# Kernel optimization log

Measured on AMD Instinct MI355X. Metric: run time of the kernel, lower is better.

The kernel has to match this reference:

```python
import jax, jax.numpy as jnp
import numpy as np

NUM_NODES = 50000

def setup_inputs() -> dict:
    key = jax.random.key(0)
    k1, k2 = jax.random.split(key)
    x = jax.random.normal(k1, (NUM_NODES, 64), dtype=jnp.float32)
    edge_index = jax.random.randint(k2, (2, 800000), 0, NUM_NODES, dtype=jnp.int64)
    return {"x": x, "edge_index": edge_index}

def reference(x, edge_index):
    # gather source-node features along edges, scatter-mean into target nodes
    row, col = edge_index[0], edge_index[1]
    num_nodes = x.shape[0]
    gathered = x[row]  # [E, D]
    summed = jax.ops.segment_sum(gathered, col, num_segments=num_nodes)  # [N, D]
    count = jax.ops.segment_sum(jnp.ones_like(col, dtype=x.dtype), col, num_segments=num_nodes)  # [N]
    # mean with divide-by-zero guard (matches torch_geometric scatter reduce='mean')
    out = summed / jnp.maximum(count, 1.0)[:, None]
    return out
```

## Files before the change

kernel.cpp:

```cpp
#include <hip/hip_runtime.h>

#define N_NODES 50000
#define DIM 64
#define NPB 32
#define NB 1563
#define NCHUNK 256
#define CAPB 1024
#define CAP 1024

typedef unsigned short ushort_t;

__device__ __forceinline__ ushort_t f32_to_bf16(float f) {
    unsigned u = __float_as_uint(f);
    u += 0x7FFFu + ((u >> 16) & 1u);
    return (ushort_t)(u >> 16);
}

__device__ __forceinline__ void acc_pair(float& a0, float& a1, unsigned u) {
    a0 += __uint_as_float(u << 16);
    a1 += __uint_as_float(u & 0xFFFF0000u);
}

__global__ void init_cursor_kernel(int* __restrict__ cursor) {
    int t = blockIdx.x * blockDim.x + threadIdx.x;
    if (t <= NB) cursor[t] = t * CAPB;
}

__global__ void binning_kernel(const float* __restrict__ xf,
                               ushort_t* __restrict__ xh,
                               const int* __restrict__ row,
                               const int* __restrict__ col,
                               int* __restrict__ cursor,
                               unsigned* __restrict__ packed,
                               int E, int chunk, int n4) {
    __shared__ int h[NB];
    __shared__ int lcur[NB];
    int c = blockIdx.x;
    int tid = threadIdx.x;
    for (int i = c * blockDim.x + tid; i < n4; i += gridDim.x * blockDim.x) {
        float4 v = *reinterpret_cast<const float4*>(xf + (size_t)i * 4);
        ushort4 hh;
        hh.x = f32_to_bf16(v.x);
        hh.y = f32_to_bf16(v.y);
        hh.z = f32_to_bf16(v.z);
        hh.w = f32_to_bf16(v.w);
        *reinterpret_cast<ushort4*>(xh + (size_t)i * 4) = hh;
    }
    for (int b = tid; b < NB; b += blockDim.x) h[b] = 0;
    __syncthreads();
    int beg = c * chunk, end = min(beg + chunk, E);
    int nfull = (end - beg) >> 2;
    for (int g = tid; g < nfull; g += blockDim.x) {
        int4 c4 = *reinterpret_cast<const int4*>(col + beg + g * 4);
        atomicAdd(&h[c4.x >> 5], 1);
        atomicAdd(&h[c4.y >> 5], 1);
        atomicAdd(&h[c4.z >> 5], 1);
        atomicAdd(&h[c4.w >> 5], 1);
    }
    for (int e = beg + nfull * 4 + tid; e < end; e += blockDim.x)
        atomicAdd(&h[col[e] >> 5], 1);
    __syncthreads();
    for (int b = tid; b < NB; b += blockDim.x) {
        int v = h[b];
        lcur[b] = (v > 0) ? atomicAdd(&cursor[b], v) : 0;
    }
    __syncthreads();
    for (int g = tid; g < nfull; g += blockDim.x) {
        int e = beg + g * 4;
        int4 d4 = *reinterpret_cast<const int4*>(col + e);
        int4 s4 = *reinterpret_cast<const int4*>(row + e);
        int p0 = atomicAdd(&lcur[d4.x >> 5], 1);
        packed[p0] = (unsigned)s4.x | ((unsigned)(d4.x & 31) << 16);
        int p1 = atomicAdd(&lcur[d4.y >> 5], 1);
        packed[p1] = (unsigned)s4.y | ((unsigned)(d4.y & 31) << 16);
        int p2 = atomicAdd(&lcur[d4.z >> 5], 1);
        packed[p2] = (unsigned)s4.z | ((unsigned)(d4.z & 31) << 16);
        int p3 = atomicAdd(&lcur[d4.w >> 5], 1);
        packed[p3] = (unsigned)s4.w | ((unsigned)(d4.w & 31) << 16);
    }
    for (int e = beg + nfull * 4 + tid; e < end; e += blockDim.x) {
        int d = col[e];
        int p = atomicAdd(&lcur[d >> 5], 1);
        packed[p] = (unsigned)row[e] | ((unsigned)(d & 31) << 16);
    }
}

template <bool BF16>
__global__ __launch_bounds__(512)
void aggregate_bucket_kernel(const float* __restrict__ xf,
                             const ushort_t* __restrict__ xh,
                             const unsigned* __restrict__ packed,
                             const int* __restrict__ cursor,
                             float* __restrict__ out) {
    __shared__ unsigned short srcs[CAP];
    __shared__ int hist[NPB];
    __shared__ int segoff[NPB];
    __shared__ int lcur[NPB];
    __shared__ int cnt_tot[NPB];

    int b = blockIdx.x;
    int tid = threadIdx.x;
    int lane = tid & 63;
    int wv = tid >> 6;
    int g8 = lane >> 3;
    int o = lane & 7;
    int seg_beg = b * CAPB;
    int seg_end = cursor[b];
    int node_base = b * NPB;
    int nnodes = min(NPB, N_NODES - node_base);

    float acc[4][8];
    #pragma unroll
    for (int r = 0; r < 4; ++r)
        #pragma unroll
        for (int k = 0; k < 8; ++k) acc[r][k] = 0.0f;
    if (tid < NPB) cnt_tot[tid] = 0;

    for (int cs = seg_beg; cs < seg_end; cs += CAP) {
        int m = min(CAP, seg_end - cs);
        __syncthreads();
        if (tid < NPB) hist[tid] = 0;
        __syncthreads();
        {
            int nf = m >> 2;
            const uint4* p4 = reinterpret_cast<const uint4*>(packed + cs);
            for (int i = tid; i < nf; i += 512) {
                uint4 v = p4[i];
                atomicAdd(&hist[v.x >> 16], 1);
                atomicAdd(&hist[v.y >> 16], 1);
                atomicAdd(&hist[v.z >> 16], 1);
                atomicAdd(&hist[v.w >> 16], 1);
            }
            for (int i = nf * 4 + tid; i < m; i += 512)
                atomicAdd(&hist[packed[cs + i] >> 16], 1);
        }
        __syncthreads();
        if (tid < NPB) {
            int v = hist[tid];
            int incl = v;
            #pragma unroll
            for (int ofs = 1; ofs < 32; ofs <<= 1) {
                int t = __shfl_up(incl, ofs);
                if (lane >= ofs) incl += t;
            }
            segoff[tid] = incl - v;
            lcur[tid] = incl - v;
            cnt_tot[tid] += v;
        }
        __syncthreads();
        for (int i = tid; i < m; i += 512) {
            unsigned v = packed[cs + i];
            int p = atomicAdd(&lcur[v >> 16], 1);
            srcs[p] = (unsigned short)(v & 0xFFFF);
        }
        __syncthreads();
        #pragma unroll
        for (int r = 0; r < 4; ++r) {
            int ln = wv * 4 + r;
            int st = segoff[ln];
            int len = hist[ln];
            int j = 0;
            for (; j + 16 <= len; j += 16) {
                int s0 = srcs[st + j + g8];
                int s1 = srcs[st + j + 8 + g8];
                if (BF16) {
                    uint4 a0 = *reinterpret_cast<const uint4*>(xh + (size_t)s0 * DIM + o * 8);
                    uint4 a1 = *reinterpret_cast<const uint4*>(xh + (size_t)s1 * DIM + o * 8);
                    acc_pair(acc[r][0], acc[r][1], a0.x);
                    acc_pair(acc[r][2], acc[r][3], a0.y);
                    acc_pair(acc[r][4], acc[r][5], a0.z);
                    acc_pair(acc[r][6], acc[r][7], a0.w);
                    acc_pair(acc[r][0], acc[r][1], a1.x);
                    acc_pair(acc[r][2], acc[r][3], a1.y);
                    acc_pair(acc[r][4], acc[r][5], a1.z);
                    acc_pair(acc[r][6], acc[r][7], a1.w);
                } else {
                    float4 u0 = *reinterpret_cast<const float4*>(xf + (size_t)s0 * DIM + o * 8);
                    float4 u1 = *reinterpret_cast<const float4*>(xf + (size_t)s0 * DIM + o * 8 + 4);
                    float4 u2 = *reinterpret_cast<const float4*>(xf + (size_t)s1 * DIM + o * 8);
                    float4 u3 = *reinterpret_cast<const float4*>(xf + (size_t)s1 * DIM + o * 8 + 4);
                    acc[r][0] += u0.x + u2.x; acc[r][1] += u0.y + u2.y;
                    acc[r][2] += u0.z + u2.z; acc[r][3] += u0.w + u2.w;
                    acc[r][4] += u1.x + u3.x; acc[r][5] += u1.y + u3.y;
                    acc[r][6] += u1.z + u3.z; acc[r][7] += u1.w + u3.w;
                }
            }
            for (; j < len; j += 8) {
                if (j + g8 < len) {
                    int s = srcs[st + j + g8];
                    if (BF16) {
                        uint4 a0 = *reinterpret_cast<const uint4*>(xh + (size_t)s * DIM + o * 8);
                        acc_pair(acc[r][0], acc[r][1], a0.x);
                        acc_pair(acc[r][2], acc[r][3], a0.y);
                        acc_pair(acc[r][4], acc[r][5], a0.z);
                        acc_pair(acc[r][6], acc[r][7], a0.w);
                    } else {
                        float4 u0 = *reinterpret_cast<const float4*>(xf + (size_t)s * DIM + o * 8);
                        float4 u1 = *reinterpret_cast<const float4*>(xf + (size_t)s * DIM + o * 8 + 4);
                        acc[r][0] += u0.x; acc[r][1] += u0.y;
                        acc[r][2] += u0.z; acc[r][3] += u0.w;
                        acc[r][4] += u1.x; acc[r][5] += u1.y;
                        acc[r][6] += u1.z; acc[r][7] += u1.w;
                    }
                }
            }
        }
    }
    __syncthreads();
    #pragma unroll
    for (int r = 0; r < 4; ++r) {
        int ln = wv * 4 + r;
        #pragma unroll
        for (int k = 0; k < 8; ++k) {
            acc[r][k] += __shfl_xor(acc[r][k], 8);
            acc[r][k] += __shfl_xor(acc[r][k], 16);
            acc[r][k] += __shfl_xor(acc[r][k], 32);
        }
        if (g8 == 0 && ln < nnodes) {
            int c = cnt_tot[ln];
            float inv = (c > 0) ? 1.0f / (float)c : 0.0f;
            float4 lo = make_float4(acc[r][0] * inv, acc[r][1] * inv,
                                    acc[r][2] * inv, acc[r][3] * inv);
            float4 hi = make_float4(acc[r][4] * inv, acc[r][5] * inv,
                                    acc[r][6] * inv, acc[r][7] * inv);
            float* op = out + (size_t)(node_base + ln) * DIM + o * 8;
            *reinterpret_cast<float4*>(op) = lo;
            *reinterpret_cast<float4*>(op + 4) = hi;
        }
    }
}

extern "C" void kernel_launch(void* const* d_in, const int* in_sizes, int n_in,
                              void* d_out, int out_size, void* d_ws, size_t ws_size,
                              hipStream_t stream) {
    const float* x = (const float*)d_in[0];
    const int* edge_index = (const int*)d_in[1];
    int E = in_sizes[1] / 2;
    const int* row = edge_index;
    const int* col = edge_index + E;
    float* out = (float*)d_out;

    int chunk = (((E + NCHUNK - 1) / NCHUNK) + 3) & ~3;
    int n4 = N_NODES * DIM / 4;

    int* cursor      = (int*)d_ws;
    unsigned* packed = (unsigned*)(cursor + 1568);
    ushort_t* xh     = (ushort_t*)(packed + (size_t)NB * CAPB);
    size_t need_bf16 = (size_t)((char*)(xh + (size_t)N_NODES * DIM) - (char*)d_ws);
    bool use_bf16 = (ws_size >= need_bf16);

    init_cursor_kernel<<<7, 256, 0, stream>>>(cursor);
    binning_kernel<<<NCHUNK, 1024, 0, stream>>>(x, xh, row, col, cursor, packed,
                                                E, chunk, use_bf16 ? n4 : 0);
    if (use_bf16)
        aggregate_bucket_kernel<true><<<NB, 512, 0, stream>>>(x, xh, packed, cursor, out);
    else
        aggregate_bucket_kernel<false><<<NB, 512, 0, stream>>>(x, xh, packed, cursor, out);
}
```

Before: 56.95 us.

## Process each bucket in a single pass and halve the binning chunk count

The aggregate kernel drops its loop over capacity chunks and assumes each bucket fits in one shared-memory chunk. Each thread keeps its at most two packed entries in registers between the histogram and the scatter passes, so they are read from global memory only once, and the per-chunk count accumulator is removed. Output is written with nontemporal scalar stores, and the binning pass uses fewer chunks. If any bucket could exceed the capacity this would be wrong, but the bucket capacity already matches CAP.

After: 52.89 us (median of 3 runs). 7.1% less time.

```diff
diff --git a/kernel.cpp b/kernel.cpp
--- a/kernel.cpp
+++ b/kernel.cpp
@@ -4,7 +4,7 @@
 #define DIM 64
 #define NPB 32
 #define NB 1563
-#define NCHUNK 256
+#define NCHUNK 128
 #define CAPB 1024
 #define CAP 1024
 
@@ -96,7 +96,6 @@
     __shared__ int hist[NPB];
     __shared__ int segoff[NPB];
     __shared__ int lcur[NPB];
-    __shared__ int cnt_tot[NPB];
 
     int b = blockIdx.x;
     int tid = threadIdx.x;
@@ -105,103 +104,89 @@
     int g8 = lane >> 3;
     int o = lane & 7;
     int seg_beg = b * CAPB;
-    int seg_end = cursor[b];
+    int m = cursor[b] - seg_beg;
     int node_base = b * NPB;
     int nnodes = min(NPB, N_NODES - node_base);
+
+    if (tid < NPB) hist[tid] = 0;
+    __syncthreads();
+
+    unsigned v0 = 0, v1 = 0;
+    int i0 = tid, i1 = tid + 512;
+    if (i0 < m) { v0 = packed[seg_beg + i0]; atomicAdd(&hist[v0 >> 16], 1); }
+    if (i1 < m) { v1 = packed[seg_beg + i1]; atomicAdd(&hist[v1 >> 16], 1); }
+    __syncthreads();
+
+    if (tid < NPB) {
+        int v = hist[tid];
+        int incl = v;
+        #pragma unroll
+        for (int ofs = 1; ofs < 32; ofs <<= 1) {
+            int t = __shfl_up(incl, ofs);
+            if (lane >= ofs) incl += t;
+        }
+        segoff[tid] = incl - v;
+        lcur[tid] = incl - v;
+    }
+    __syncthreads();
+
+    if (i0 < m) { int p = atomicAdd(&lcur[v0 >> 16], 1); srcs[p] = (unsigned short)(v0 & 0xFFFF); }
+    if (i1 < m) { int p = atomicAdd(&lcur[v1 >> 16], 1); srcs[p] = (unsigned short)(v1 & 0xFFFF); }
+    __syncthreads();
 
     float acc[4][8];
     #pragma unroll
     for (int r = 0; r < 4; ++r)
         #pragma unroll
         for (int k = 0; k < 8; ++k) acc[r][k] = 0.0f;
-    if (tid < NPB) cnt_tot[tid] = 0;
-
-    for (int cs = seg_beg; cs < seg_end; cs += CAP) {
-        int m = min(CAP, seg_end - cs);
-        __syncthreads();
-        if (tid < NPB) hist[tid] = 0;
-        __syncthreads();
-        {
-            int nf = m >> 2;
-            const uint4* p4 = reinterpret_cast<const uint4*>(packed + cs);
-            for (int i = tid; i < nf; i += 512) {
-                uint4 v = p4[i];
-                atomicAdd(&hist[v.x >> 16], 1);
-                atomicAdd(&hist[v.y >> 16], 1);
-                atomicAdd(&hist[v.z >> 16], 1);
-                atomicAdd(&hist[v.w >> 16], 1);
+
+    #pragma unroll
+    for (int r = 0; r < 4; ++r) {
+        int ln = wv * 4 + r;
+        int st = segoff[ln];
+        int len = hist[ln];
+        int j = 0;
+        for (; j + 16 <= len; j += 16) {
+            int s0 = srcs[st + j + g8];
+            int s1 = srcs[st + j + 8 + g8];
+            if (BF16) {
+                uint4 a0 = *reinterpret_cast<const uint4*>(xh + (size_t)s0 * DIM + o * 8);
+                uint4 a1 = *reinterpret_cast<const uint4*>(xh + (size_t)s1 * DIM + o * 8);
+                acc_pair(acc[r][0], acc[r][1], a0.x);
+                acc_pair(acc[r][2], acc[r][3], a0.y);
+                acc_pair(acc[r][4], acc[r][5], a0.z);
+                acc_pair(acc[r][6], acc[r][7], a0.w);
+                acc_pair(acc[r][0], acc[r][1], a1.x);
+                acc_pair(acc[r][2], acc[r][3], a1.y);
+                acc_pair(acc[r][4], acc[r][5], a1.z);
+                acc_pair(acc[r][6], acc[r][7], a1.w);
+            } else {
+                float4 u0 = *reinterpret_cast<const float4*>(xf + (size_t)s0 * DIM + o * 8);
+                float4 u1 = *reinterpret_cast<const float4*>(xf + (size_t)s0 * DIM + o * 8 + 4);
+                float4 u2 = *reinterpret_cast<const float4*>(xf + (size_t)s1 * DIM + o * 8);
+                float4 u3 = *reinterpret_cast<const float4*>(xf + (size_t)s1 * DIM + o * 8 + 4);
+                acc[r][0] += u0.x + u2.x; acc[r][1] += u0.y + u2.y;
+                acc[r][2] += u0.z + u2.z; acc[r][3] += u0.w + u2.w;
+                acc[r][4] += u1.x + u3.x; acc[r][5] += u1.y + u3.y;
+                acc[r][6] += u1.z + u3.z; acc[r][7] += u1.w + u3.w;
             }
-            for (int i = nf * 4 + tid; i < m; i += 512)
-                atomicAdd(&hist[packed[cs + i] >> 16], 1);
-        }
-        __syncthreads();
-        if (tid < NPB) {
-            int v = hist[tid];
-            int incl = v;
-            #pragma unroll
-            for (int ofs = 1; ofs < 32; ofs <<= 1) {
-                int t = __shfl_up(incl, ofs);
-                if (lane >= ofs) incl += t;
-            }
-            segoff[tid] = incl - v;
-            lcur[tid] = incl - v;
-            cnt_tot[tid] += v;
-        }
-        __syncthreads();
-        for (int i = tid; i < m; i += 512) {
-            unsigned v = packed[cs + i];
-            int p = atomicAdd(&lcur[v >> 16], 1);
-            srcs[p] = (unsigned short)(v & 0xFFFF);
-        }
-        __syncthreads();
-        #pragma unroll
-        for (int r = 0; r < 4; ++r) {
-            int ln = wv * 4 + r;
-            int st = segoff[ln];
-            int len = hist[ln];
-            int j = 0;
-            for (; j + 16 <= len; j += 16) {
-                int s0 = srcs[st + j + g8];
-                int s1 = srcs[st + j + 8 + g8];
+        }
+        for (; j < len; j += 8) {
+            if (j + g8 < len) {
+                int s = srcs[st + j + g8];
                 if (BF16) {
-                    uint4 a0 = *reinterpret_cast<const uint4*>(xh + (size_t)s0 * DIM + o * 8);
-                    uint4 a1 = *reinterpret_cast<const uint4*>(xh + (size_t)s1 * DIM + o * 8);
+                    uint4 a0 = *reinterpret_cast<const uint4*>(xh + (size_t)s * DIM + o * 8);
                     acc_pair(acc[r][0], acc[r][1], a0.x);
                     acc_pair(acc[r][2], acc[r][3], a0.y);
                     acc_pair(acc[r][4], acc[r][5], a0.z);
                     acc_pair(acc[r][6], acc[r][7], a0.w);
-                    acc_pair(acc[r][0], acc[r][1], a1.x);
-                    acc_pair(acc[r][2], acc[r][3], a1.y);
-                    acc_pair(acc[r][4], acc[r][5], a1.z);
-                    acc_pair(acc[r][6], acc[r][7], a1.w);
                 } else {
-                    float4 u0 = *reinterpret_cast<const float4*>(xf + (size_t)s0 * DIM + o * 8);
-                    float4 u1 = *reinterpret_cast<const float4*>(xf + (size_t)s0 * DIM + o * 8 + 4);
-                    float4 u2 = *reinterpret_cast<const float4*>(xf + (size_t)s1 * DIM + o * 8);
-                    float4 u3 = *reinterpret_cast<const float4*>(xf + (size_t)s1 * DIM + o * 8 + 4);
-                    acc[r][0] += u0.x + u2.x; acc[r][1] += u0.y + u2.y;
-                    acc[r][2] += u0.z + u2.z; acc[r][3] += u0.w + u2.w;
-                    acc[r][4] += u1.x + u3.x; acc[r][5] += u1.y + u3.y;
-                    acc[r][6] += u1.z + u3.z; acc[r][7] += u1.w + u3.w;
-                }
-            }
-            for (; j < len; j += 8) {
-                if (j + g8 < len) {
-                    int s = srcs[st + j + g8];
-                    if (BF16) {
-                        uint4 a0 = *reinterpret_cast<const uint4*>(xh + (size_t)s * DIM + o * 8);
-                        acc_pair(acc[r][0], acc[r][1], a0.x);
-                        acc_pair(acc[r][2], acc[r][3], a0.y);
-                        acc_pair(acc[r][4], acc[r][5], a0.z);
-                        acc_pair(acc[r][6], acc[r][7], a0.w);
-                    } else {
-                        float4 u0 = *reinterpret_cast<const float4*>(xf + (size_t)s * DIM + o * 8);
-                        float4 u1 = *reinterpret_cast<const float4*>(xf + (size_t)s * DIM + o * 8 + 4);
-                        acc[r][0] += u0.x; acc[r][1] += u0.y;
-                        acc[r][2] += u0.z; acc[r][3] += u0.w;
-                        acc[r][4] += u1.x; acc[r][5] += u1.y;
-                        acc[r][6] += u1.z; acc[r][7] += u1.w;
-                    }
+                    float4 u0 = *reinterpret_cast<const float4*>(xf + (size_t)s * DIM + o * 8);
+                    float4 u1 = *reinterpret_cast<const float4*>(xf + (size_t)s * DIM + o * 8 + 4);
+                    acc[r][0] += u0.x; acc[r][1] += u0.y;
+                    acc[r][2] += u0.z; acc[r][3] += u0.w;
+                    acc[r][4] += u1.x; acc[r][5] += u1.y;
+                    acc[r][6] += u1.z; acc[r][7] += u1.w;
                 }
             }
         }
@@ -217,15 +202,12 @@
             acc[r][k] += __shfl_xor(acc[r][k], 32);
         }
         if (g8 == 0 && ln < nnodes) {
-            int c = cnt_tot[ln];
+            int c = hist[ln];
             float inv = (c > 0) ? 1.0f / (float)c : 0.0f;
-            float4 lo = make_float4(acc[r][0] * inv, acc[r][1] * inv,
-                                    acc[r][2] * inv, acc[r][3] * inv);
-            float4 hi = make_float4(acc[r][4] * inv, acc[r][5] * inv,
-                                    acc[r][6] * inv, acc[r][7] * inv);
             float* op = out + (size_t)(node_base + ln) * DIM + o * 8;
-            *reinterpret_cast<float4*>(op) = lo;
-            *reinterpret_cast<float4*>(op + 4) = hi;
+            #pragma unroll
+            for (int k = 0; k < 8; ++k)
+                __builtin_nontemporal_store(acc[r][k] * inv, op + k);
         }
     }
 }
```
